# Kernel optimization log

Hardware: AMD Instinct MI355X
Metric: run time of the kernel (lower is better)

## Reference

```python
import jax, jax.numpy as jnp
import numpy as np

B, S, D, R, H, NI, NP, NO, K = 2, 2048, 1024, 1024, 8, 8, 32, 8, 3
DH = R // H


def setup_inputs() -> dict:
    key = jax.random.key(0)
    ks = jax.random.split(key, 32)
    rn = lambda k, shp, s=1.0: jax.random.normal(k, shp, jnp.float32) * s
    nrm = lambda v: v / (jnp.linalg.norm(v, axis=-1, keepdims=True) + 1e-8)
    w = 1.0 / np.sqrt(D).astype(np.float32)
    inp = {
        'x': rn(ks[0], (B, S, D)),
        'mask': jnp.tril(jnp.ones((S, S), bool))[None, None],  # causal [1,1,S,S]
        'Wr_in': rn(ks[1], (NI, D), w), 'Wr_proc': rn(ks[2], (NP, D), w), 'Wr_out': rn(ks[3], (NO, D), w),
        'WrO_in': rn(ks[4], (NI, R), w), 'WrO_proc': rn(ks[5], (NP, R), w), 'WrO_out': rn(ks[6], (NO, R), w),
        'Wq_in': rn(ks[7], (NI, D, R), w), 'vq': nrm(rn(ks[8], (NP, R))), 'Wq_out': rn(ks[9], (NO, R, D), w),
        'Wk_in': rn(ks[10], (NI, D, R), w), 'vk': nrm(rn(ks[11], (NP, R))), 'Wk_out': rn(ks[12], (NO, R, D), w),
        'Wv_in': rn(ks[13], (NI, D, R), w), 'vv': nrm(rn(ks[14], (NP, R))), 'Wv_out': rn(ks[15], (NO, R, D), w),
        # circuit_O = NeuronCircuit(rank, d_model): dims swapped
        'Wo_in': rn(ks[16], (NI, R, D), w), 'vo': nrm(rn(ks[17], (NP, D))), 'Wo_out': rn(ks[18], (NO, D, R), w),
    }
    return inp


def _router(x, Wi, Wp, Wo, k):
    in_w = jax.nn.softmax(x @ Wi.T, axis=-1)            # [B,S,NI]
    _, proc_idx = jax.lax.top_k(x @ Wp.T, k)            # [B,S,k]
    out_w = jax.nn.softmax(x @ Wo.T, axis=-1)           # [B,S,NO]
    return in_w, proc_idx, out_w


def _circuit(x, Win, vproc, Wout, in_w, proc_idx, out_w):
    # soft input mix: d_in -> r
    h = jnp.einsum('bsd,ndr,bsn->bsr', x, Win, in_w)
    # k sequential Householder reflections with gathered vectors
    v = vproc[proc_idx]                                 # [B,S,k,r]
    v = v / jnp.sqrt(jnp.sum(v * v, axis=-1, keepdims=True) + 1e-8)
    for i in range(v.shape[2]):
        vi = v[:, :, i, :]
        h = h - 2.0 * vi * jnp.sum(h * vi, axis=-1, keepdims=True)
    # soft output mix: r -> d_out
    return jnp.einsum('bsr,nrd,bsn->bsd', h, Wout, out_w)


def reference(x, mask, Wr_in, Wr_proc, Wr_out, WrO_in, WrO_proc, WrO_out,
              Wq_in, vq, Wq_out, Wk_in, vk, Wk_out, Wv_in, vv, Wv_out,
              Wo_in, vo, Wo_out):
    in_w, pidx, out_w = _router(x, Wr_in, Wr_proc, Wr_out, K)
    Q = _circuit(x, Wq_in, vq, Wq_out, in_w, pidx, out_w)   # [B,S,R]
    Kt = _circuit(x, Wk_in, vk, Wk_out, in_w, pidx, out_w)
    V = _circuit(x, Wv_in, vv, Wv_out, in_w, pidx, out_w)
    q = Q.reshape(B, S, H, DH).transpose(0, 2, 1, 3)
    k = Kt.reshape(B, S, H, DH).transpose(0, 2, 1, 3)
    v = V.reshape(B, S, H, DH).transpose(0, 2, 1, 3)
    scores = jnp.einsum('bhqd,bhkd->bhqk', q, k) / np.sqrt(DH).astype(np.float32)
    scores = jnp.where(mask, scores, jnp.float32(-1e9))
    p = jax.nn.softmax(scores, axis=-1)
    o = jnp.einsum('bhqk,bhkd->bhqd', p, v)
    o = o.transpose(0, 2, 1, 3).reshape(B, S, R)
    in_wO, pidxO, out_wO = _router(o, WrO_in, WrO_proc, WrO_out, K)
    out = _circuit(o, Wo_in, vo, Wo_out, in_wO, pidxO, out_wO)  # [B,S,D]
    return out
```

## Files before the change

kernel.cpp:

```cpp
#include <hip/hip_runtime.h>


typedef __attribute__((ext_vector_type(4))) float f32x4;
typedef _Float16 f16x8 __attribute__((ext_vector_type(8)));
typedef _Float16 f16x4 __attribute__((ext_vector_type(4)));

static constexpr int S_LEN  = 2048;
static constexpr int TOK    = 4096;
static constexpr int DMODEL = 1024;
static constexpr int KDIM   = 8192;

__device__ __forceinline__ void async16(const void* g, void* l) {
  __builtin_amdgcn_global_load_lds(
      (const __attribute__((address_space(1))) void*)g,
      (__attribute__((address_space(3))) void*)l, 16, 0, 0);
}

__global__ __launch_bounds__(256) void transpose_split(const float* __restrict__ W,
                                                       _Float16* __restrict__ Th,
                                                       _Float16* __restrict__ Tl) {
  __shared__ float tbuf[64][65];
  const int tid = threadIdx.x;
  const int k0 = blockIdx.x * 64, n0 = blockIdx.y * 64;
#pragma unroll
  for (int j = 0; j < 4; ++j) {
    int ci = tid + 256 * j;
    int r = ci >> 4, c4 = (ci & 15) * 4;
    float4 v = *(const float4*)&W[(size_t)(k0 + r) * DMODEL + n0 + c4];
    tbuf[r][c4 + 0] = v.x; tbuf[r][c4 + 1] = v.y;
    tbuf[r][c4 + 2] = v.z; tbuf[r][c4 + 3] = v.w;
  }
  __syncthreads();
#pragma unroll
  for (int j = 0; j < 2; ++j) {
    int ci = tid + 256 * j;
    int nl = ci >> 3, k8 = (ci & 7) * 8;
    f16x8 hv, lv;
#pragma unroll
    for (int e = 0; e < 8; ++e) {
      float v = tbuf[k8 + e][nl];
      _Float16 hh = (_Float16)v;
      hv[e] = hh;
      lv[e] = (_Float16)(v - (float)hh);
    }
    size_t off = (size_t)(n0 + nl) * KDIM + k0 + k8;
    *(f16x8*)&Th[off] = hv;
    *(f16x8*)&Tl[off] = lv;
  }
}

__global__ __launch_bounds__(256) void router_kernel(const float* __restrict__ X,
                                                     const float* __restrict__ Wi,
                                                     const float* __restrict__ Wp,
                                                     const float* __restrict__ Wo,
                                                     float* __restrict__ in_w,
                                                     float* __restrict__ out_w,
                                                     int* __restrict__ pidx,
                                                     _Float16* __restrict__ Xh,
                                                     _Float16* __restrict__ Xl) {
  __shared__ float xs[1024];
  __shared__ double lg[48];
  const int t = blockIdx.x, tid = threadIdx.x;
  const int wid = tid >> 6, lane = tid & 63;
#pragma unroll
  for (int j = 0; j < 4; ++j) {
    int d = tid + 256 * j;
    xs[d] = X[(size_t)t * DMODEL + d];
  }
  __syncthreads();
  for (int i = wid; i < 48; i += 4) {
    const float* wrow = (i < 8)  ? Wi + (size_t)i * DMODEL
                      : (i < 40) ? Wp + (size_t)(i - 8) * DMODEL
                                 : Wo + (size_t)(i - 40) * DMODEL;
    double s = 0.0;
#pragma unroll
    for (int j = 0; j < 16; ++j) { int d = lane + 64 * j; s += (double)xs[d] * (double)wrow[d]; }
#pragma unroll
    for (int mm = 32; mm >= 1; mm >>= 1) s += __shfl_xor(s, mm);
    if (lane == 0) lg[i] = s;
  }
  __syncthreads();
  if (tid == 0) {
    float l[8], m;
    for (int i = 0; i < 8; ++i) l[i] = (float)lg[i];
    m = l[0];
    for (int i = 1; i < 8; ++i) m = fmaxf(m, l[i]);
    float e[8], su = 0.f;
    for (int i = 0; i < 8; ++i) { e[i] = expf(l[i] - m); su += e[i]; }
    for (int i = 0; i < 8; ++i) in_w[t * 8 + i] = e[i] / su;
  } else if (tid == 64) {
    float l[8], m;
    for (int i = 0; i < 8; ++i) l[i] = (float)lg[40 + i];
    m = l[0];
    for (int i = 1; i < 8; ++i) m = fmaxf(m, l[i]);
    float e[8], su = 0.f;
    for (int i = 0; i < 8; ++i) { e[i] = expf(l[i] - m); su += e[i]; }
    for (int i = 0; i < 8; ++i) out_w[t * 8 + i] = e[i] / su;
  } else if (tid == 128) {
    unsigned used = 0;
    for (int j = 0; j < 3; ++j) {
      double best = -1e300; int bi = 0;
      for (int i = 0; i < 32; ++i)
        if (!((used >> i) & 1u) && lg[8 + i] > best) { best = lg[8 + i]; bi = i; }
      used |= 1u << bi;
      pidx[t * 3 + j] = bi;
    }
  }
  if (Xh != nullptr) {
#pragma unroll
    for (int j = 0; j < 4; ++j) {
      int d = tid + 256 * j;
      float v = xs[d];
      _Float16 hh = (_Float16)v;
      Xh[(size_t)t * DMODEL + d] = hh;
      Xl[(size_t)t * DMODEL + d] = (_Float16)(v - (float)hh);
    }
  }
}

__global__ __launch_bounds__(256) void reflect4_kernel(const float* __restrict__ Pa,
                                                       const float* __restrict__ Pb,
                                                       const float* __restrict__ Pc,
                                                       const float* __restrict__ Pd,
                                                       const int* __restrict__ pidx,
                                                       const float* __restrict__ vtab,
                                                       _Float16* __restrict__ Hh,
                                                       _Float16* __restrict__ Hl) {
  __shared__ float red[8];
  const int t = blockIdx.x, tid = threadIdx.x;
  const int wid = tid >> 6, lane = tid & 63;
  size_t gi = (size_t)t * DMODEL + tid * 4;
  float4 ha = *(const float4*)&Pa[gi];
  float4 hb = *(const float4*)&Pb[gi];
  float4 hc = *(const float4*)&Pc[gi];
  float4 hd = *(const float4*)&Pd[gi];
  float4 h = {ha.x + hb.x + hc.x + hd.x, ha.y + hb.y + hc.y + hd.y,
              ha.z + hb.z + hc.z + hd.z, ha.w + hb.w + hc.w + hd.w};
  for (int i = 0; i < 3; ++i) {
    int idx = pidx[t * 3 + i];
    float4 vi = *(const float4*)&vtab[(size_t)idx * DMODEL + tid * 4];
    float hv = h.x * vi.x + h.y * vi.y + h.z * vi.z + h.w * vi.w;
    float vv = vi.x * vi.x + vi.y * vi.y + vi.z * vi.z + vi.w * vi.w;
#pragma unroll
    for (int mm = 32; mm >= 1; mm >>= 1) { hv += __shfl_xor(hv, mm); vv += __shfl_xor(vv, mm); }
    if (lane == 0) { red[wid] = hv; red[4 + wid] = vv; }
    __syncthreads();
    float dot = red[0] + red[1] + red[2] + red[3];
    float vn  = red[4] + red[5] + red[6] + red[7];
    __syncthreads();
    float c = 2.f * dot / (vn + 1e-8f);
    h.x -= c * vi.x; h.y -= c * vi.y; h.z -= c * vi.z; h.w -= c * vi.w;
  }
  float a[4] = {h.x, h.y, h.z, h.w};
  f16x4 hv4, lv4;
#pragma unroll
  for (int e = 0; e < 4; ++e) {
    _Float16 hh = (_Float16)a[e];
    hv4[e] = hh;
    lv4[e] = (_Float16)(a[e] - (float)hh);
  }
  *(f16x4*)&Hh[gi] = hv4;
  *(f16x4*)&Hl[gi] = lv4;
}

__global__ __launch_bounds__(256) void reduce4_planes(const float* __restrict__ a,
                                                      const float* __restrict__ b,
                                                      const float* __restrict__ c,
                                                      const float* __restrict__ d,
                                                      _Float16* __restrict__ Dh,
                                                      _Float16* __restrict__ Dl) {
  size_t i = ((size_t)blockIdx.x * 256 + threadIdx.x) * 4;
  float4 va = *(const float4*)&a[i];
  float4 vb = *(const float4*)&b[i];
  float4 vc = *(const float4*)&c[i];
  float4 vd = *(const float4*)&d[i];
  float s[4] = {va.x + vb.x + vc.x + vd.x, va.y + vb.y + vc.y + vd.y,
                va.z + vb.z + vc.z + vd.z, va.w + vb.w + vc.w + vd.w};
  f16x4 hv, lv;
#pragma unroll
  for (int e = 0; e < 4; ++e) {
    _Float16 hh = (_Float16)s[e];
    hv[e] = hh;
    lv[e] = (_Float16)(s[e] - (float)hh);
  }
  *(f16x4*)&Dh[i] = hv;
  *(f16x4*)&Dl[i] = lv;
}

__global__ __launch_bounds__(256) void reduce4_f32(const float* __restrict__ a,
                                                   const float* __restrict__ b,
                                                   const float* __restrict__ c,
                                                   const float* __restrict__ d,
                                                   float* __restrict__ o) {
  size_t i = ((size_t)blockIdx.x * 256 + threadIdx.x) * 4;
  float4 va = *(const float4*)&a[i];
  float4 vb = *(const float4*)&b[i];
  float4 vc = *(const float4*)&c[i];
  float4 vd = *(const float4*)&d[i];
  float4 vo = {va.x + vb.x + vc.x + vd.x, va.y + vb.y + vc.y + vd.y,
               va.z + vb.z + vc.z + vd.z, va.w + vb.w + vc.w + vd.w};
  *(float4*)&o[i] = vo;
}

template <bool FAST>
__global__ __launch_bounds__(512, 2) void gemm_planes(const _Float16* __restrict__ Ahp,
                                                      const _Float16* __restrict__ Alp,
                                                      const float* __restrict__ wmix,
                                                      const _Float16* __restrict__ Bh,
                                                      const _Float16* __restrict__ Bl,
                                                      float* __restrict__ C0,
                                                      float* __restrict__ C1,
                                                      float* __restrict__ C2,
                                                      float* __restrict__ C3) {
  __shared__ _Float16 sAh[256 * 32];
  __shared__ _Float16 sBh[256 * 32];
  __shared__ _Float16 sAl[FAST ? 8 : 256 * 32];
  __shared__ _Float16 sBl[FAST ? 8 : 256 * 32];
  __shared__ float sWr[256 * 2];
  const int tid = threadIdx.x;
  const int wid = tid >> 6, lane = tid & 63;
  const int l16 = lane & 15, lhi = lane >> 4;
  const int wr = wid >> 2, wc = wid & 3;
  const int fid = blockIdx.x + (blockIdx.y << 4) + (blockIdx.z << 6);
  const int wg  = ((fid & 7) << 5) + (fid >> 3);
  const int bm = (wg & 15) * 256;
  const int bn = ((wg >> 4) & 3) * 256;
  const int kz = wg >> 6;
  const int kbase = kz * 2048, nb = kz * 2;
  float* __restrict__ Cp = (kz == 0) ? C0 : (kz == 1) ? C1 : (kz == 2) ? C2 : C3;

  {
    int row = tid >> 1, p = tid & 1;
    const float* w = &wmix[(size_t)(bm + row) * 8 + nb];
    sWr[tid] = p ? w[1] : w[0] / w[1];
  }

  f32x4 acc[8][4];
#pragma unroll
  for (int i = 0; i < 8; ++i)
#pragma unroll
    for (int j = 0; j < 4; ++j) { f32x4 z = {0.f, 0.f, 0.f, 0.f}; acc[i][j] = z; }

  for (int kt = 0; kt < 2048; kt += 32) {
    const int kg = kbase + kt, d0 = kg & 1023;
#pragma unroll
    for (int j = 0; j < 2; ++j) {
      int ci = tid + 512 * j;
      int row = ci >> 2, jc = ci & 3;
      int jcs = jc ^ ((row >> 1) & 3);
      size_t ga = (size_t)(bm + row) * DMODEL + d0 + jcs * 8;
      size_t gb = (size_t)(bn + row) * KDIM + kg + jcs * 8;
      async16(&Ahp[ga], &sAh[ci * 8]);
      async16(&Bh[gb],  &sBh[ci * 8]);
      if (!FAST) {
        async16(&Alp[ga], &sAl[ci * 8]);
        async16(&Bl[gb],  &sBl[ci * 8]);
      }
    }
    __syncthreads();
    f16x8 b_h[4], b_l[4];
#pragma unroll
    for (int ni = 0; ni < 4; ++ni) {
      int row = wc * 64 + ni * 16 + l16;
      int idx = row * 32 + ((lhi ^ ((row >> 1) & 3)) * 8);
      b_h[ni] = *(const f16x8*)&sBh[idx];
      if (!FAST) b_l[ni] = *(const f16x8*)&sBl[idx];
    }
#pragma unroll
    for (int mi = 0; mi < 8; ++mi) {
      int rowa = wr * 128 + mi * 16 + l16;
      int idxa = rowa * 32 + ((lhi ^ ((rowa >> 1) & 3)) * 8);
      f16x8 a_h = *(const f16x8*)&sAh[idxa];
      f16x8 a_l;
      if (!FAST) a_l = *(const f16x8*)&sAl[idxa];
#pragma unroll
      for (int ni = 0; ni < 4; ++ni) {
        f32x4 a = acc[mi][ni];
        a = __builtin_amdgcn_mfma_f32_16x16x32_f16(a_h, b_h[ni], a, 0, 0, 0);
        if (!FAST) {
          a = __builtin_amdgcn_mfma_f32_16x16x32_f16(a_h, b_l[ni], a, 0, 0, 0);
          a = __builtin_amdgcn_mfma_f32_16x16x32_f16(a_l, b_h[ni], a, 0, 0, 0);
        }
        acc[mi][ni] = a;
      }
    }
    __syncthreads();
    if (kt == 992) {
#pragma unroll
      for (int mi = 0; mi < 8; ++mi)
#pragma unroll
        for (int r = 0; r < 4; ++r) {
          float s = sWr[(wr * 128 + mi * 16 + lhi * 4 + r) * 2];
#pragma unroll
          for (int ni = 0; ni < 4; ++ni) acc[mi][ni][r] *= s;
        }
    }
  }
#pragma unroll
  for (int mi = 0; mi < 8; ++mi)
#pragma unroll
    for (int r = 0; r < 4; ++r) {
      int rowl = wr * 128 + mi * 16 + lhi * 4 + r;
      float s = sWr[rowl * 2 + 1];
#pragma unroll
      for (int ni = 0; ni < 4; ++ni) {
        int col = bn + wc * 64 + ni * 16 + l16;
        Cp[(size_t)(bm + rowl) * DMODEL + col] = acc[mi][ni][r] * s;
      }
    }
}

__global__ __launch_bounds__(256) void vtrans4_kernel(const float* __restrict__ Va,
                                                      const float* __restrict__ Vb,
                                                      const float* __restrict__ Vc,
                                                      const float* __restrict__ Vd,
                                                      _Float16* __restrict__ Vth,
                                                      _Float16* __restrict__ Vtl) {
  __shared__ float tbuf[64][65];
  const int tid = threadIdx.x;
  const int t0 = blockIdx.x * 64, d0 = blockIdx.y * 64, bh = blockIdx.z;
  const int b = bh >> 3, h = bh & 7;
#pragma unroll
  for (int j = 0; j < 4; ++j) {
    int ci = tid + 256 * j;
    int r = ci >> 4, c4 = (ci & 15) * 4;
    size_t g = (size_t)(b * S_LEN + t0 + r) * DMODEL + h * 128 + d0 + c4;
    float4 va = *(const float4*)&Va[g];
    float4 vb = *(const float4*)&Vb[g];
    float4 vc = *(const float4*)&Vc[g];
    float4 vd = *(const float4*)&Vd[g];
    tbuf[r][c4 + 0] = va.x + vb.x + vc.x + vd.x;
    tbuf[r][c4 + 1] = va.y + vb.y + vc.y + vd.y;
    tbuf[r][c4 + 2] = va.z + vb.z + vc.z + vd.z;
    tbuf[r][c4 + 3] = va.w + vb.w + vc.w + vd.w;
  }
  __syncthreads();
#pragma unroll
  for (int j = 0; j < 4; ++j) {
    int ci = tid + 256 * j;
    int r = ci >> 4, c4 = (ci & 15) * 4;
    float s[4] = {tbuf[c4 + 0][r], tbuf[c4 + 1][r], tbuf[c4 + 2][r], tbuf[c4 + 3][r]};
    f16x4 hv, lv;
#pragma unroll
    for (int e = 0; e < 4; ++e) {
      _Float16 hh = (_Float16)s[e];
      hv[e] = hh;
      lv[e] = (_Float16)(s[e] - (float)hh);
    }
    size_t o = ((size_t)bh * 128 + d0 + r) * S_LEN + t0 + c4;
    *(f16x4*)&Vth[o] = hv;
    *(f16x4*)&Vtl[o] = lv;
  }
}

__global__ __launch_bounds__(256) void attn_kernel(const _Float16* __restrict__ Qh,
                                                   const _Float16* __restrict__ Ql,
                                                   const _Float16* __restrict__ Kh,
                                                   const _Float16* __restrict__ Kl,
                                                   const _Float16* __restrict__ Vth,
                                                   const _Float16* __restrict__ Vtl,
                                                   float* __restrict__ O,
                                                   _Float16* __restrict__ Oh) {
  __shared__ _Float16 sKh[32 * 128], sKl[32 * 128];
  __shared__ _Float16 sVh[128 * 32], sVl[128 * 32];
  __shared__ _Float16 sPh[4 * 16 * 32], sPl[4 * 16 * 32];
  const int tid = threadIdx.x;
  const int wid = tid >> 6, lane = tid & 63;
  const int l16 = lane & 15, lhi = lane >> 4;
  const int qt = (gridDim.x - 1) - blockIdx.x;
  const int bh = blockIdx.y;
  const int b = bh >> 3, h = bh & 7;
  const size_t qkbase = (size_t)b * S_LEN * DMODEL + h * 128;
  const float scale = 0.08838834764831845f;

  const int qrow = qt * 64 + wid * 16 + l16;
  const size_t qoff = qkbase + (size_t)qrow * DMODEL;
  f16x8 qh[4], ql[4];
#pragma unroll
  for (int kk = 0; kk < 4; ++kk) {
    qh[kk] = *(const f16x8*)&Qh[qoff + kk * 32 + lhi * 8];
    ql[kk] = *(const f16x8*)&Ql[qoff + kk * 32 + lhi * 8];
  }

  f32x4 of[8];
#pragma unroll
  for (int i = 0; i < 8; ++i) { f32x4 z = {0.f, 0.f, 0.f, 0.f}; of[i] = z; }
  float m_[4], l_[4];
#pragma unroll
  for (int r = 0; r < 4; ++r) { m_[r] = -1e30f; l_[r] = 0.f; }

  const int ntw = qt * 2 + 1 + (wid >> 1);
  const int NT  = qt * 2 + 2;

  for (int kt = 0; kt < NT; ++kt) {
    __syncthreads();
#pragma unroll
    for (int j = 0; j < 2; ++j) {
      int ci = tid + 256 * j;
      int k = ci >> 4, c = ci & 15;
      int cs = c ^ (k & 7);
      size_t g = qkbase + (size_t)(kt * 32 + k) * DMODEL + cs * 8;
      async16(&Kh[g], &sKh[k * 128 + c * 8]);
      async16(&Kl[g], &sKl[k * 128 + c * 8]);
    }
#pragma unroll
    for (int j = 0; j < 2; ++j) {
      int ci = tid + 256 * j;
      int d = ci >> 2, c = ci & 3;
      int cs = c ^ ((d >> 1) & 3);
      size_t g = ((size_t)bh * 128 + d) * S_LEN + kt * 32 + cs * 8;
      async16(&Vth[g], &sVh[d * 32 + c * 8]);
      async16(&Vtl[g], &sVl[d * 32 + c * 8]);
    }
    __syncthreads();

    if (kt < ntw) {
      f32x4 s0 = {0.f, 0.f, 0.f, 0.f}, s1 = {0.f, 0.f, 0.f, 0.f};
#pragma unroll
      for (int kk = 0; kk < 4; ++kk) {
        int col = (kk * 32 + lhi * 8);
        int i0 = l16 * 128 + (col ^ ((l16 & 7) * 8));
        int i1 = (16 + l16) * 128 + (col ^ (((16 + l16) & 7) * 8));
        f16x8 kb0h = *(const f16x8*)&sKh[i0];
        f16x8 kb0l = *(const f16x8*)&sKl[i0];
        f16x8 kb1h = *(const f16x8*)&sKh[i1];
        f16x8 kb1l = *(const f16x8*)&sKl[i1];
        s0 = __builtin_amdgcn_mfma_f32_16x16x32_f16(qh[kk], kb0h, s0, 0, 0, 0);
        s0 = __builtin_amdgcn_mfma_f32_16x16x32_f16(qh[kk], kb0l, s0, 0, 0, 0);
        s0 = __builtin_amdgcn_mfma_f32_16x16x32_f16(ql[kk], kb0h, s0, 0, 0, 0);
        s1 = __builtin_amdgcn_mfma_f32_16x16x32_f16(qh[kk], kb1h, s1, 0, 0, 0);
        s1 = __builtin_amdgcn_mfma_f32_16x16x32_f16(qh[kk], kb1l, s1, 0, 0, 0);
        s1 = __builtin_amdgcn_mfma_f32_16x16x32_f16(ql[kk], kb1h, s1, 0, 0, 0);
      }
      const int qg = qt * 64 + wid * 16 + (lane >> 4) * 4;
      if (kt == ntw - 1) {
#pragma unroll
        for (int r = 0; r < 4; ++r) {
          int q = qg + r;
          int k0 = kt * 32 + l16, k1 = k0 + 16;
          s0[r] = (k0 <= q) ? s0[r] * scale : -1e30f;
          s1[r] = (k1 <= q) ? s1[r] * scale : -1e30f;
        }
      } else {
#pragma unroll
        for (int r = 0; r < 4; ++r) { s0[r] *= scale; s1[r] *= scale; }
      }
      float p0[4], p1[4], fr[4];
#pragma unroll
      for (int r = 0; r < 4; ++r) {
        float rm = fmaxf(s0[r], s1[r]);
        rm = fmaxf(rm, __shfl_xor(rm, 1));
        rm = fmaxf(rm, __shfl_xor(rm, 2));
        rm = fmaxf(rm, __shfl_xor(rm, 4));
        rm = fmaxf(rm, __shfl_xor(rm, 8));
        float mn = fmaxf(m_[r], rm);
        fr[r] = __expf(m_[r] - mn);
        m_[r] = mn;
        p0[r] = __expf(s0[r] - mn);
        p1[r] = __expf(s1[r] - mn);
        float rs = p0[r] + p1[r];
        rs += __shfl_xor(rs, 1);
        rs += __shfl_xor(rs, 2);
        rs += __shfl_xor(rs, 4);
        rs += __shfl_xor(rs, 8);
        l_[r] = l_[r] * fr[r] + rs;
      }
#pragma unroll
      for (int i = 0; i < 8; ++i)
#pragma unroll
        for (int r = 0; r < 4; ++r) of[i][r] *= fr[r];
#pragma unroll
      for (int r = 0; r < 4; ++r) {
        int q = (lane >> 4) * 4 + r;
        int swz = ((q >> 1) & 3) * 8;
        int c0 = l16, c1 = 16 + l16;
        _Float16 h0 = (_Float16)p0[r];
        _Float16 h1 = (_Float16)p1[r];
        sPh[wid * 512 + q * 32 + (c0 ^ swz)] = h0;
        sPl[wid * 512 + q * 32 + (c0 ^ swz)] = (_Float16)(p0[r] - (float)h0);
        sPh[wid * 512 + q * 32 + (c1 ^ swz)] = h1;
        sPl[wid * 512 + q * 32 + (c1 ^ swz)] = (_Float16)(p1[r] - (float)h1);
      }
      int pidxr = wid * 512 + l16 * 32 + ((lhi * 8) ^ (((l16 >> 1) & 3) * 8));
      f16x8 pah = *(const f16x8*)&sPh[pidxr];
      f16x8 pal = *(const f16x8*)&sPl[pidxr];
#pragma unroll
      for (int d16 = 0; d16 < 8; ++d16) {
        int d = d16 * 16 + l16;
        int vidx = d * 32 + ((lhi * 8) ^ (((d >> 1) & 3) * 8));
        f16x8 vbh = *(const f16x8*)&sVh[vidx];
        f16x8 vbl = *(const f16x8*)&sVl[vidx];
        f32x4 a = of[d16];
        a = __builtin_amdgcn_mfma_f32_16x16x32_f16(pah, vbh, a, 0, 0, 0);
        a = __builtin_amdgcn_mfma_f32_16x16x32_f16(pah, vbl, a, 0, 0, 0);
        a = __builtin_amdgcn_mfma_f32_16x16x32_f16(pal, vbh, a, 0, 0, 0);
        of[d16] = a;
      }
    }
  }
  float inv[4];
#pragma unroll
  for (int r = 0; r < 4; ++r) inv[r] = 1.f / l_[r];
  const int qg = qt * 64 + wid * 16 + (lane >> 4) * 4;
#pragma unroll
  for (int d16 = 0; d16 < 8; ++d16)
#pragma unroll
    for (int r = 0; r < 4; ++r) {
      float val = of[d16][r] * inv[r];
      size_t gi = qkbase + (size_t)(qg + r) * DMODEL + d16 * 16 + l16;
      O[gi] = val;
      Oh[gi] = (_Float16)val;
    }
}

extern "C" void kernel_launch(void* const* d_in, const int* in_sizes, int n_in,
                              void* d_out, int out_size, void* d_ws, size_t ws_size,
                              hipStream_t stream) {
  (void)in_sizes; (void)n_in; (void)out_size;
  const float* x        = (const float*)d_in[0];
  const float* Wr_in    = (const float*)d_in[2];
  const float* Wr_proc  = (const float*)d_in[3];
  const float* Wr_out   = (const float*)d_in[4];
  const float* WrO_in   = (const float*)d_in[5];
  const float* WrO_proc = (const float*)d_in[6];
  const float* WrO_out  = (const float*)d_in[7];
  const float* Wq_in    = (const float*)d_in[8];
  const float* vq       = (const float*)d_in[9];
  const float* Wq_out   = (const float*)d_in[10];
  const float* Wk_in    = (const float*)d_in[11];
  const float* vk       = (const float*)d_in[12];
  const float* Wk_out   = (const float*)d_in[13];
  const float* Wv_in    = (const float*)d_in[14];
  const float* vv       = (const float*)d_in[15];
  const float* Wv_out   = (const float*)d_in[16];
  const float* Wo_in    = (const float*)d_in[17];
  const float* vo       = (const float*)d_in[18];
  const float* Wo_out   = (const float*)d_in[19];

  char* wsbase = (char*)d_ws;
  size_t off = 0;
  auto carve = [&](size_t bytes) -> void* {
    void* r = wsbase + off;
    off = (off + bytes + 255) & ~(size_t)255;
    return r;
  };
  const size_t WBYTES = (size_t)KDIM * DMODEL * 2;
  const size_t PBYTES = (size_t)TOK * DMODEL * 2;
  const size_t HBYTES = (size_t)TOK * DMODEL * 4;
  _Float16* WTh = (_Float16*)carve(WBYTES);
  _Float16* WTl = (_Float16*)carve(WBYTES);
  _Float16* Xh  = (_Float16*)carve(PBYTES);
  _Float16* Xl  = (_Float16*)carve(PBYTES);
  _Float16* Hh  = (_Float16*)carve(PBYTES);
  _Float16* Hl  = (_Float16*)carve(PBYTES);
  float* P0 = (float*)carve(HBYTES);
  float* P1 = (float*)carve(HBYTES);
  float* P2 = (float*)carve(HBYTES);
  _Float16* Qph = (_Float16*)carve(PBYTES);
  _Float16* Qpl = (_Float16*)carve(PBYTES);
  _Float16* Kph = (_Float16*)carve(PBYTES);
  _Float16* Kpl = (_Float16*)carve(PBYTES);
  float* iw1 = (float*)carve((size_t)TOK * 8 * 4);
  float* ow1 = (float*)carve((size_t)TOK * 8 * 4);
  float* iw2 = (float*)carve((size_t)TOK * 8 * 4);
  float* ow2 = (float*)carve((size_t)TOK * 8 * 4);
  int* pi1 = (int*)carve((size_t)TOK * 3 * 4);
  int* pi2 = (int*)carve((size_t)TOK * 3 * 4);

  if (off > ws_size) {
    hipMemsetAsync(d_out, 0, (size_t)out_size * 4, stream);
    return;
  }

  float*    Pd  = (float*)d_out;
  float*    PQ  = (float*)Qph;
  float*    PX  = (float*)Xh;
  _Float16* Vth = WTh;
  _Float16* Vtl = WTh + (size_t)TOK * DMODEL;
  float*    Ofp = P0;
  _Float16* Ohp = (_Float16*)P1;

  const dim3 blk(256);
  const dim3 gblk(512);
  const dim3 tgrid(KDIM / 64, DMODEL / 64);
  const dim3 ggrid(TOK / 256, DMODEL / 256, 4);
  const dim3 rgrid(TOK * DMODEL / (256 * 4));
  const dim3 vgrid(S_LEN / 64, 2, 16);
  const dim3 agrid(S_LEN / 64, 16);

  router_kernel<<<TOK, blk, 0, stream>>>(x, Wr_in, Wr_proc, Wr_out, iw1, ow1, pi1, Xh, Xl);

  transpose_split<<<tgrid, blk, 0, stream>>>(Wq_in, WTh, WTl);
  gemm_planes<false><<<ggrid, gblk, 0, stream>>>(Xh, Xl, iw1, WTh, WTl, P0, P1, P2, Pd);
  reflect4_kernel<<<TOK, blk, 0, stream>>>(P0, P1, P2, Pd, pi1, vq, Hh, Hl);
  transpose_split<<<tgrid, blk, 0, stream>>>(Wq_out, WTh, WTl);
  gemm_planes<false><<<ggrid, gblk, 0, stream>>>(Hh, Hl, ow1, WTh, WTl, P0, P1, P2, Pd);
  reduce4_planes<<<rgrid, blk, 0, stream>>>(P0, P1, P2, Pd, Qph, Qpl);

  transpose_split<<<tgrid, blk, 0, stream>>>(Wk_in, WTh, WTl);
  gemm_planes<false><<<ggrid, gblk, 0, stream>>>(Xh, Xl, iw1, WTh, WTl, P0, P1, P2, Pd);
  reflect4_kernel<<<TOK, blk, 0, stream>>>(P0, P1, P2, Pd, pi1, vk, Hh, Hl);
  transpose_split<<<tgrid, blk, 0, stream>>>(Wk_out, WTh, WTl);
  gemm_planes<false><<<ggrid, gblk, 0, stream>>>(Hh, Hl, ow1, WTh, WTl, P0, P1, P2, Pd);
  reduce4_planes<<<rgrid, blk, 0, stream>>>(P0, P1, P2, Pd, Kph, Kpl);

  transpose_split<<<tgrid, blk, 0, stream>>>(Wv_in, WTh, WTl);
  gemm_planes<false><<<ggrid, gblk, 0, stream>>>(Xh, Xl, iw1, WTh, WTl, P0, P1, P2, Pd);
  reflect4_kernel<<<TOK, blk, 0, stream>>>(P0, P1, P2, Pd, pi1, vv, Hh, Hl);
  transpose_split<<<tgrid, blk, 0, stream>>>(Wv_out, WTh, WTl);
  gemm_planes<false><<<ggrid, gblk, 0, stream>>>(Hh, Hl, ow1, WTh, WTl, P0, P1, P2, Pd);
  vtrans4_kernel<<<vgrid, blk, 0, stream>>>(P0, P1, P2, Pd, Vth, Vtl);

  attn_kernel<<<agrid, blk, 0, stream>>>(Qph, Qpl, Kph, Kpl, Vth, Vtl, Ofp, Ohp);

  router_kernel<<<TOK, blk, 0, stream>>>(Ofp, WrO_in, WrO_proc, WrO_out, iw2, ow2, pi2,
                                         nullptr, nullptr);
  transpose_split<<<tgrid, blk, 0, stream>>>(Wo_in, WTh, WTl);
  gemm_planes<true><<<ggrid, gblk, 0, stream>>>(Ohp, Ohp, iw2, WTh, WTl, PX, P0, P2, Pd);
  reflect4_kernel<<<TOK, blk, 0, stream>>>(PX, P0, P2, Pd, pi2, vo, Hh, Hl);
  transpose_split<<<tgrid, blk, 0, stream>>>(Wo_out, WTh, WTl);
  gemm_planes<true><<<ggrid, gblk, 0, stream>>>(Hh, Hh, ow2, WTh, WTl, P0, P1, P2, PQ);
  reduce4_f32<<<rgrid, blk, 0, stream>>>(P0, P1, P2, PQ, (float*)d_out);
}
```

Baseline: 1.747 ms.

## Double-buffer LDS tiles in gemm_planes and skip unused low-plane weight writes

The plane GEMM loop is restructured into a two-stage software pipeline. Each iteration issues the async global-to-LDS loads for tile k+1, then waits with an explicit vmcnt so only the current tile must have landed, and computes on it, with raised wave priority during the MFMA section. This is meant to hide global load latency behind MFMA work. The cost is double the LDS footprint per block, which for the non-FAST variant (about 128KB) may stop two blocks from sharing a CU. Separately, the transpose kernel no longer writes the low fp16 plane when it is called for the FAST-path weights, which never read it, saving some memory traffic.

Result: faster. 1.645 ms (-5.8%).

```diff
diff --git a/kernel.cpp b/kernel.cpp
--- a/kernel.cpp
+++ b/kernel.cpp
@@ -45,7 +45,7 @@
     }
     size_t off = (size_t)(n0 + nl) * KDIM + k0 + k8;
     *(f16x8*)&Th[off] = hv;
-    *(f16x8*)&Tl[off] = lv;
+    if (Tl != nullptr) *(f16x8*)&Tl[off] = lv;
   }
 }
 
@@ -212,10 +212,10 @@
                                                       float* __restrict__ C1,
                                                       float* __restrict__ C2,
                                                       float* __restrict__ C3) {
-  __shared__ _Float16 sAh[256 * 32];
-  __shared__ _Float16 sBh[256 * 32];
-  __shared__ _Float16 sAl[FAST ? 8 : 256 * 32];
-  __shared__ _Float16 sBl[FAST ? 8 : 256 * 32];
+  __shared__ _Float16 sAh[2][256 * 32];
+  __shared__ _Float16 sBh[2][256 * 32];
+  __shared__ _Float16 sAl[2][FAST ? 8 : 256 * 32];
+  __shared__ _Float16 sBl[2][FAST ? 8 : 256 * 32];
   __shared__ float sWr[256 * 2];
   const int tid = threadIdx.x;
   const int wid = tid >> 6, lane = tid & 63;
@@ -241,7 +241,7 @@
 #pragma unroll
     for (int j = 0; j < 4; ++j) { f32x4 z = {0.f, 0.f, 0.f, 0.f}; acc[i][j] = z; }
 
-  for (int kt = 0; kt < 2048; kt += 32) {
+  auto STAGE = [&](int buf, int kt) {
     const int kg = kbase + kt, d0 = kg & 1023;
 #pragma unroll
     for (int j = 0; j < 2; ++j) {
@@ -250,42 +250,55 @@
       int jcs = jc ^ ((row >> 1) & 3);
       size_t ga = (size_t)(bm + row) * DMODEL + d0 + jcs * 8;
       size_t gb = (size_t)(bn + row) * KDIM + kg + jcs * 8;
-      async16(&Ahp[ga], &sAh[ci * 8]);
-      async16(&Bh[gb],  &sBh[ci * 8]);
-      if (!FAST) {
-        async16(&Alp[ga], &sAl[ci * 8]);
-        async16(&Bl[gb],  &sBl[ci * 8]);
-      }
-    }
-    __syncthreads();
+      async16(&Ahp[ga], &sAh[buf][ci * 8]);
+      async16(&Bh[gb],  &sBh[buf][ci * 8]);
+      if constexpr (!FAST) {
+        async16(&Alp[ga], &sAl[buf][ci * 8]);
+        async16(&Bl[gb],  &sBl[buf][ci * 8]);
+      }
+    }
+  };
+
+  auto COMPUTE = [&](int buf) {
+    __builtin_amdgcn_s_setprio(1);
     f16x8 b_h[4], b_l[4];
 #pragma unroll
     for (int ni = 0; ni < 4; ++ni) {
       int row = wc * 64 + ni * 16 + l16;
       int idx = row * 32 + ((lhi ^ ((row >> 1) & 3)) * 8);
-      b_h[ni] = *(const f16x8*)&sBh[idx];
-      if (!FAST) b_l[ni] = *(const f16x8*)&sBl[idx];
+      b_h[ni] = *(const f16x8*)&sBh[buf][idx];
+      if constexpr (!FAST) b_l[ni] = *(const f16x8*)&sBl[buf][idx];
     }
 #pragma unroll
     for (int mi = 0; mi < 8; ++mi) {
       int rowa = wr * 128 + mi * 16 + l16;
       int idxa = rowa * 32 + ((lhi ^ ((rowa >> 1) & 3)) * 8);
-      f16x8 a_h = *(const f16x8*)&sAh[idxa];
+      f16x8 a_h = *(const f16x8*)&sAh[buf][idxa];
       f16x8 a_l;
-      if (!FAST) a_l = *(const f16x8*)&sAl[idxa];
+      if constexpr (!FAST) a_l = *(const f16x8*)&sAl[buf][idxa];
 #pragma unroll
       for (int ni = 0; ni < 4; ++ni) {
         f32x4 a = acc[mi][ni];
         a = __builtin_amdgcn_mfma_f32_16x16x32_f16(a_h, b_h[ni], a, 0, 0, 0);
-        if (!FAST) {
+        if constexpr (!FAST) {
           a = __builtin_amdgcn_mfma_f32_16x16x32_f16(a_h, b_l[ni], a, 0, 0, 0);
           a = __builtin_amdgcn_mfma_f32_16x16x32_f16(a_l, b_h[ni], a, 0, 0, 0);
         }
         acc[mi][ni] = a;
       }
     }
-    __syncthreads();
-    if (kt == 992) {
+    __builtin_amdgcn_s_setprio(0);
+  };
+
+  STAGE(0, 0);
+  for (int t = 0; t < 63; ++t) {
+    STAGE((t + 1) & 1, (t + 1) * 32);
+    if constexpr (FAST) asm volatile("s_waitcnt vmcnt(4)" ::: "memory");
+    else                asm volatile("s_waitcnt vmcnt(8)" ::: "memory");
+    __builtin_amdgcn_s_barrier();
+    __builtin_amdgcn_sched_barrier(0);
+    COMPUTE(t & 1);
+    if (t == 31) {
 #pragma unroll
       for (int mi = 0; mi < 8; ++mi)
 #pragma unroll
@@ -295,7 +308,13 @@
           for (int ni = 0; ni < 4; ++ni) acc[mi][ni][r] *= s;
         }
     }
-  }
+    __builtin_amdgcn_s_barrier();
+  }
+  asm volatile("s_waitcnt vmcnt(0)" ::: "memory");
+  __builtin_amdgcn_s_barrier();
+  __builtin_amdgcn_sched_barrier(0);
+  COMPUTE(1);
+
 #pragma unroll
   for (int mi = 0; mi < 8; ++mi)
 #pragma unroll
@@ -615,10 +634,10 @@
 
   router_kernel<<<TOK, blk, 0, stream>>>(Ofp, WrO_in, WrO_proc, WrO_out, iw2, ow2, pi2,
                                          nullptr, nullptr);
-  transpose_split<<<tgrid, blk, 0, stream>>>(Wo_in, WTh, WTl);
-  gemm_planes<true><<<ggrid, gblk, 0, stream>>>(Ohp, Ohp, iw2, WTh, WTl, PX, P0, P2, Pd);
+  transpose_split<<<tgrid, blk, 0, stream>>>(Wo_in, WTh, nullptr);
+  gemm_planes<true><<<ggrid, gblk, 0, stream>>>(Ohp, Ohp, iw2, WTh, WTh, PX, P0, P2, Pd);
   reflect4_kernel<<<TOK, blk, 0, stream>>>(PX, P0, P2, Pd, pi2, vo, Hh, Hl);
-  transpose_split<<<tgrid, blk, 0, stream>>>(Wo_out, WTh, WTl);
-  gemm_planes<true><<<ggrid, gblk, 0, stream>>>(Hh, Hh, ow2, WTh, WTl, P0, P1, P2, PQ);
+  transpose_split<<<tgrid, blk, 0, stream>>>(Wo_out, WTh, nullptr);
+  gemm_planes<true><<<ggrid, gblk, 0, stream>>>(Hh, Hh, ow2, WTh, WTh, P0, P1, P2, PQ);
   reduce4_f32<<<rgrid, blk, 0, stream>>>(P0, P1, P2, PQ, (float*)d_out);
 }
```
